# Kernel tuning notes

Measured on AMD Instinct MI355X. Metric: run time of the kernel, lower is better.

Reference implementation:

```python
import jax, jax.numpy as jnp
import numpy as np

V = 49688; D = 128; Hd = 256; DM = 2 * Hd; FF = 4 * Hd; NH = 4
B = 256; O = 32; L = 32

def _ln(x, g, b, eps=1e-5):
    m = x.mean(-1, keepdims=True)
    v = x.var(-1, keepdims=True)
    return (x - m) / jnp.sqrt(v + eps) * g + b

def _mha(x, in_w, in_b, out_w, out_b, nh):
    Bx, S, E = x.shape
    hd = E // nh
    qkv = x @ in_w.T + in_b
    q, k, v = jnp.split(qkv, 3, axis=-1)
    sp = lambda t: t.reshape(Bx, S, nh, hd).transpose(0, 2, 1, 3)
    q, k, v = sp(q), sp(k), sp(v)
    s = jnp.einsum('bhqd,bhkd->bhqk', q, k) / jnp.sqrt(jnp.asarray(hd, x.dtype))
    o = jnp.einsum('bhqk,bhkd->bhqd', jax.nn.softmax(s, -1), v)
    o = o.transpose(0, 2, 1, 3).reshape(Bx, S, E)
    return o @ out_w.T + out_b

def _gru_dir(x, wih, whh, bih, bhh):
    Bx, T, _ = x.shape
    H = whh.shape[1]
    def step(h, xt):
        gi = xt @ wih.T + bih
        gh = h @ whh.T + bhh
        ir, iz, inn = jnp.split(gi, 3, -1)
        hr, hz, hn = jnp.split(gh, 3, -1)
        r = jax.nn.sigmoid(ir + hr)
        z = jax.nn.sigmoid(iz + hz)
        n = jnp.tanh(inn + r * hn)
        h = (1 - z) * n + z * h
        return h, h
    _, hs = jax.lax.scan(step, jnp.zeros((Bx, H), x.dtype), jnp.swapaxes(x, 0, 1))
    return jnp.swapaxes(hs, 0, 1)

def setup_inputs():
    key = jax.random.key(0)
    it = iter(jax.random.split(key, 48))
    def nrm(shape, s=0.05):
        return jax.random.normal(next(it), shape, jnp.float32) * s
    inp = {}
    inp['order_history'] = jax.random.randint(next(it), (B, O, L), 0, V + 1)
    inp['days_between'] = jax.random.uniform(next(it), (B, O - 1), jnp.float32) * 30.0
    inp['days_since_last'] = jax.random.uniform(next(it), (B,), jnp.float32) * 30.0
    inp['emb'] = nrm((V + 1, D), 1.0).at[0].set(0.0)  # padding_idx=0 -> zero row
    inp['a_in_w'] = nrm((3 * D, D)); inp['a_in_b'] = jnp.zeros((3 * D,))
    inp['a_out_w'] = nrm((D, D)); inp['a_out_b'] = jnp.zeros((D,))
    for d in ('f', 'b'):
        inp['g_wih_' + d] = nrm((3 * Hd, D)); inp['g_whh_' + d] = nrm((3 * Hd, Hd))
        inp['g_bih_' + d] = jnp.zeros((3 * Hd,)); inp['g_bhh_' + d] = jnp.zeros((3 * Hd,))
    inp['t_in_w'] = nrm((3 * DM, DM)); inp['t_in_b'] = jnp.zeros((3 * DM,))
    inp['t_out_w'] = nrm((DM, DM)); inp['t_out_b'] = jnp.zeros((DM,))
    inp['t_ln1_g'] = jnp.ones((DM,)); inp['t_ln1_b'] = jnp.zeros((DM,))
    inp['t_ff1_w'] = nrm((FF, DM)); inp['t_ff1_b'] = jnp.zeros((FF,))
    inp['t_ff2_w'] = nrm((DM, FF)); inp['t_ff2_b'] = jnp.zeros((DM,))
    inp['t_ln2_g'] = jnp.ones((DM,)); inp['t_ln2_b'] = jnp.zeros((DM,))
    inp['te1_w'] = nrm((Hd // 4, 2)); inp['te1_b'] = jnp.zeros((Hd // 4,))
    inp['te_ln1_g'] = jnp.ones((Hd // 4,)); inp['te_ln1_b'] = jnp.zeros((Hd // 4,))
    inp['te2_w'] = nrm((Hd // 2, Hd // 4)); inp['te2_b'] = jnp.zeros((Hd // 2,))
    inp['te_ln2_g'] = jnp.ones((Hd // 2,)); inp['te_ln2_b'] = jnp.zeros((Hd // 2,))
    inp['c_w'] = nrm((Hd, 2 * Hd + Hd // 2)); inp['c_b'] = jnp.zeros((Hd,))
    inp['c_ln_g'] = jnp.ones((Hd,)); inp['c_ln_b'] = jnp.zeros((Hd,))
    return inp

def reference(order_history, days_between, days_since_last, emb, a_in_w, a_in_b, a_out_w, a_out_b, g_wih_f, g_whh_f, g_bih_f, g_bhh_f, g_wih_b, g_whh_b, g_bih_b, g_bhh_b, t_in_w, t_in_b, t_out_w, t_out_b, t_ln1_g, t_ln1_b, t_ff1_w, t_ff1_b, t_ff2_w, t_ff2_b, t_ln2_g, t_ln2_b, te1_w, te1_b, te_ln1_g, te_ln1_b, te2_w, te2_b, te_ln2_g, te_ln2_b, c_w, c_b, c_ln_g, c_ln_b):
    Bx, Ox, Lx = order_history.shape
    # per-order item self-attention, batched over all (user, order) pairs
    x = emb[order_history].reshape(Bx * Ox, Lx, -1)                  # [B*O, L, D]
    x = _mha(x, a_in_w, a_in_b, a_out_w, a_out_b, NH)
    order_emb = x.mean(1).reshape(Bx, Ox, -1)                        # [B, O, D]
    # bidirectional GRU over the order sequence
    hf = _gru_dir(order_emb, g_wih_f, g_whh_f, g_bih_f, g_bhh_f)
    hb = _gru_dir(order_emb[:, ::-1], g_wih_b, g_whh_b, g_bih_b, g_bhh_b)[:, ::-1]
    g = jnp.concatenate([hf, hb], -1)                                # [B, O, 2H]
    # post-LN TransformerEncoderLayer (relu, dropout in eval mode)
    a = _mha(g, t_in_w, t_in_b, t_out_w, t_out_b, NH)
    g = _ln(g + a, t_ln1_g, t_ln1_b)
    f = jax.nn.relu(g @ t_ff1_w.T + t_ff1_b) @ t_ff2_w.T + t_ff2_b
    g = _ln(g + f, t_ln2_g, t_ln2_b)
    enc = g.mean(1)                                                  # [B, 2H]
    # temporal features: only days_mean and recency are used (std computed but unused in original)
    feats = jnp.stack([days_between.mean(1), days_since_last], 1)    # [B, 2]
    te = jax.nn.relu(_ln(feats @ te1_w.T + te1_b, te_ln1_g, te_ln1_b))
    te = jax.nn.relu(_ln(te @ te2_w.T + te2_b, te_ln2_g, te_ln2_b))  # [B, H/2]
    out = jax.nn.relu(_ln(jnp.concatenate([enc, te], 1) @ c_w.T + c_b, c_ln_g, c_ln_b))
    return out                                                       # [B, H]
```

## Files before the change

### kernel.cpp

```cpp
#include <hip/hip_runtime.h>
#include <hip/hip_bf16.h>
#include <math.h>

typedef __hip_bfloat16 bf16;
typedef __attribute__((ext_vector_type(8))) short short8v;
typedef __attribute__((ext_vector_type(4))) short short4v;
typedef __attribute__((ext_vector_type(4))) float float4v;
#define MFMA16 __builtin_amdgcn_mfma_f32_16x16x32_bf16

__device__ __forceinline__ float us2f(unsigned short u) {
  union { unsigned u; float f; } c; c.u = ((unsigned)u) << 16; return c.f;
}
__device__ __forceinline__ unsigned short f2us(float f) {
  return __bfloat16_as_ushort(__float2bfloat16(f));
}

__device__ __forceinline__ float dot_ff(const float* __restrict__ x,
                                        const float* __restrict__ w, int K) {
  const float4* xp = reinterpret_cast<const float4*>(x);
  const float4* wp = reinterpret_cast<const float4*>(w);
  float acc = 0.f;
  const int n = K >> 2;
  for (int i = 0; i < n; ++i) {
    float4 a = xp[i], b = wp[i];
    acc += a.x*b.x + a.y*b.y + a.z*b.z + a.w*b.w;
  }
  return acc;
}

__device__ __forceinline__ float sigm(float x) { return 1.f / (1.f + __expf(-x)); }
__device__ __forceinline__ float tanh_fast(float x) {
  x = fminf(fmaxf(x, -15.f), 15.f);
  float e = __expf(2.f * x);
  return (e - 1.f) / (e + 1.f);
}

__global__ void k_canary(float* __restrict__ out) {
  out[blockIdx.x * 256 + threadIdx.x] = 100.0f;
}

__global__ __launch_bounds__(256) void k_cvt(
    const float* __restrict__ a_in_w, const float* __restrict__ t_in_w,
    const float* __restrict__ t_out_w, const float* __restrict__ t_ff1w,
    const float* __restrict__ t_ff2w, const float* __restrict__ a_out_w,
    const float* __restrict__ emb,
    unsigned short* __restrict__ awb, unsigned short* __restrict__ twb,
    unsigned short* __restrict__ pwb, unsigned short* __restrict__ f1wb,
    unsigned short* __restrict__ f2wb, unsigned short* __restrict__ awb2,
    unsigned short* __restrict__ embb)
{
  int i = blockIdx.x * 256 + threadIdx.x;
  if (i < 1590048) {
    float4 e4 = *reinterpret_cast<const float4*>(emb + (size_t)i * 4);
    short4v s; s[0] = f2us(e4.x); s[1] = f2us(e4.y); s[2] = f2us(e4.z); s[3] = f2us(e4.w);
    *reinterpret_cast<short4v*>(embb + (size_t)i * 4) = s;
  }
  if (i < 49152)  awb[i] = f2us(a_in_w[i]);
  if (i < 786432) twb[i] = f2us(t_in_w[i]);
  if (i < 262144) pwb[i] = f2us(t_out_w[i]);
  if (i < 524288) f1wb[i] = f2us(t_ff1w[i]);
  if (i < 524288) f2wb[i] = f2us(t_ff2w[i]);
  if (i < 16384)  awb2[i] = f2us(a_out_w[i]);
}

__global__ __launch_bounds__(256) void k_gru_wb(
    const float* __restrict__ wih_f, const float* __restrict__ whh_f,
    const float* __restrict__ wih_b, const float* __restrict__ whh_b,
    unsigned short* __restrict__ whhb, unsigned short* __restrict__ wihb)
{
  int i = blockIdx.x * 256 + threadIdx.x;
  if (i >= 393216) return;
  int dir = i / 196608, r = i % 196608;
  whhb[i] = f2us((dir ? whh_b : whh_f)[r]);
  if (r < 98304) wihb[dir * 98304 + r] = f2us((dir ? wih_b : wih_f)[r]);
}

__global__ __launch_bounds__(256, 5) void k_order_attn(
    const int* __restrict__ oh, const unsigned short* __restrict__ embb,
    const unsigned short* __restrict__ awb, const float* __restrict__ in_b,
    const unsigned short* __restrict__ awb2, const float* __restrict__ out_b,
    unsigned short* __restrict__ oeb)
{
  const int bo = blockIdx.x;
  const int tid = threadIdx.x;
  __shared__ alignas(16) unsigned short regA[32 * 136];
  __shared__ alignas(16) unsigned short qb[32 * 136];
  __shared__ alignas(16) unsigned short kb[32 * 136];
  unsigned short* xs = regA;
  unsigned short* vT = regA;
  unsigned short* ob = qb;
  unsigned short* pb = kb;

  const int lane = tid & 63, wave = tid >> 6;
  const int l15 = lane & 15, quad = lane >> 4;

  for (int i = tid; i < 512; i += 256) {
    int t = i >> 4, c8 = (i & 15) << 3;
    int id = oh[bo * 32 + t];
    *reinterpret_cast<short8v*>(xs + t * 136 + c8) =
        *reinterpret_cast<const short8v*>(embb + (size_t)id * 128 + c8);
  }
  __syncthreads();
  short8v af[2][4];
#pragma unroll
  for (int mt = 0; mt < 2; ++mt)
#pragma unroll
    for (int kc = 0; kc < 4; ++kc)
      af[mt][kc] = *reinterpret_cast<const short8v*>(
          xs + (mt * 16 + l15) * 136 + kc * 32 + quad * 8);
  __syncthreads();
  for (int ni = 0; ni < 6; ++ni) {
    const int j = (wave + ni * 4) * 16 + l15;
    const unsigned short* wrow = awb + (size_t)j * 128;
    float4v acc0 = {0.f, 0.f, 0.f, 0.f}, acc1 = {0.f, 0.f, 0.f, 0.f};
#pragma unroll
    for (int kc = 0; kc < 4; ++kc) {
      short8v bfr = *reinterpret_cast<const short8v*>(wrow + kc * 32 + quad * 8);
      acc0 = MFMA16(af[0][kc], bfr, acc0, 0, 0, 0);
      acc1 = MFMA16(af[1][kc], bfr, acc1, 0, 0, 0);
    }
    const float bj = in_b[j];
    const int jj = j & 127;
    if (j < 256) {
      unsigned short* dst = (j < 128) ? qb : kb;
#pragma unroll
      for (int r = 0; r < 4; ++r) {
        int t0 = quad * 4 + r;
        dst[t0 * 136 + jj] = f2us(acc0[r] + bj);
        dst[(t0 + 16) * 136 + jj] = f2us(acc1[r] + bj);
      }
    } else {
      short4v s0, s1;
#pragma unroll
      for (int r = 0; r < 4; ++r) { s0[r] = f2us(acc0[r] + bj); s1[r] = f2us(acc1[r] + bj); }
      *reinterpret_cast<short4v*>(vT + jj * 32 + quad * 4) = s0;
      *reinterpret_cast<short4v*>(vT + jj * 32 + 16 + quad * 4) = s1;
    }
  }
  __syncthreads();
  {
    const int h = wave;
    const float scale1 = 0.17677669529663687f;
    short8v qf[2], kf[2];
#pragma unroll
    for (int mt = 0; mt < 2; ++mt)
      qf[mt] = *reinterpret_cast<const short8v*>(qb + (mt * 16 + l15) * 136 + h * 32 + quad * 8);
#pragma unroll
    for (int nt = 0; nt < 2; ++nt)
      kf[nt] = *reinterpret_cast<const short8v*>(kb + (nt * 16 + l15) * 136 + h * 32 + quad * 8);
    float4v sacc[2][2];
#pragma unroll
    for (int mt = 0; mt < 2; ++mt)
#pragma unroll
      for (int nt = 0; nt < 2; ++nt) {
        sacc[mt][nt] = (float4v){0.f, 0.f, 0.f, 0.f};
        sacc[mt][nt] = MFMA16(qf[mt], kf[nt], sacc[mt][nt], 0, 0, 0);
      }
    __syncthreads();
#pragma unroll
    for (int mt = 0; mt < 2; ++mt)
#pragma unroll
      for (int r = 0; r < 4; ++r) {
        float e0 = __expf(sacc[mt][0][r] * scale1);
        float e1 = __expf(sacc[mt][1][r] * scale1);
        int row = h * 32 + mt * 16 + quad * 4 + r;
        pb[row * 32 + l15] = f2us(e0);
        pb[row * 32 + 16 + l15] = f2us(e1);
      }
    short8v ones;
#pragma unroll
    for (int i = 0; i < 8; ++i) ones[i] = (short)0x3F80;
    short8v pf[2], vf[2];
#pragma unroll
    for (int mt = 0; mt < 2; ++mt)
      pf[mt] = *reinterpret_cast<const short8v*>(pb + (h * 32 + mt * 16 + l15) * 32 + quad * 8);
    float4v sums[2];
#pragma unroll
    for (int mt = 0; mt < 2; ++mt) {
      sums[mt] = (float4v){0.f, 0.f, 0.f, 0.f};
      sums[mt] = MFMA16(pf[mt], ones, sums[mt], 0, 0, 0);
    }
#pragma unroll
    for (int nt = 0; nt < 2; ++nt)
      vf[nt] = *reinterpret_cast<const short8v*>(vT + (h * 32 + nt * 16 + l15) * 32 + quad * 8);
    float4v oacc[2][2];
#pragma unroll
    for (int mt = 0; mt < 2; ++mt)
#pragma unroll
      for (int nt = 0; nt < 2; ++nt) {
        oacc[mt][nt] = (float4v){0.f, 0.f, 0.f, 0.f};
        oacc[mt][nt] = MFMA16(pf[mt], vf[nt], oacc[mt][nt], 0, 0, 0);
      }
#pragma unroll
    for (int mt = 0; mt < 2; ++mt)
#pragma unroll
      for (int r = 0; r < 4; ++r) {
        int t = mt * 16 + quad * 4 + r;
        float inv = 1.f / sums[mt][r];
#pragma unroll
        for (int nt = 0; nt < 2; ++nt)
          ob[t * 136 + h * 32 + nt * 16 + l15] = f2us(oacc[mt][nt][r] * inv);
      }
  }
  __syncthreads();
  {
    float4v acc[2][2];
#pragma unroll
    for (int mt = 0; mt < 2; ++mt)
#pragma unroll
      for (int nt = 0; nt < 2; ++nt) acc[mt][nt] = (float4v){0.f, 0.f, 0.f, 0.f};
#pragma unroll
    for (int kc = 0; kc < 4; ++kc) {
      short8v af0 = *reinterpret_cast<const short8v*>(ob + l15 * 136 + kc * 32 + quad * 8);
      short8v af1 = *reinterpret_cast<const short8v*>(ob + (16 + l15) * 136 + kc * 32 + quad * 8);
#pragma unroll
      for (int nt = 0; nt < 2; ++nt) {
        int j = (wave * 2 + nt) * 16 + l15;
        short8v bfr = *reinterpret_cast<const short8v*>(awb2 + (size_t)j * 128 + kc * 32 + quad * 8);
        acc[0][nt] = MFMA16(af0, bfr, acc[0][nt], 0, 0, 0);
        acc[1][nt] = MFMA16(af1, bfr, acc[1][nt], 0, 0, 0);
      }
    }
#pragma unroll
    for (int nt = 0; nt < 2; ++nt) {
      float part = 0.f;
#pragma unroll
      for (int mt = 0; mt < 2; ++mt)
#pragma unroll
        for (int r = 0; r < 4; ++r) part += acc[mt][nt][r];
      part += __shfl_xor(part, 16);
      part += __shfl_xor(part, 32);
      if (quad == 0) {
        int j = (wave * 2 + nt) * 16 + l15;
        oeb[(size_t)bo * 128 + j] = f2us(part * (1.f / 32.f) + out_b[j]);
      }
    }
  }
}

__global__ __launch_bounds__(256, 2) void k_gru_gi(
    const unsigned short* __restrict__ oeb, const unsigned short* __restrict__ wihb,
    unsigned short* __restrict__ gi)
{
  const int row0 = blockIdx.x * 32, tid = threadIdx.x;
  __shared__ alignas(16) unsigned short xs[32 * 136];
  for (int i = tid; i < 512; i += 256) {
    int t = i >> 4, c8 = (i & 15) << 3;
    *reinterpret_cast<short8v*>(xs + t * 136 + c8) =
        *reinterpret_cast<const short8v*>(oeb + (size_t)(row0 + t) * 128 + c8);
  }
  __syncthreads();
  const int lane = tid & 63, wave = tid >> 6;
  const int l15 = lane & 15, quad = lane >> 4;
  short8v af[2][4];
#pragma unroll
  for (int mt = 0; mt < 2; ++mt)
#pragma unroll
    for (int kc = 0; kc < 4; ++kc)
      af[mt][kc] = *reinterpret_cast<const short8v*>(
          xs + (mt * 16 + l15) * 136 + kc * 32 + quad * 8);
  for (int ni = 0; ni < 24; ++ni) {
    int col = (wave + ni * 4) * 16 + l15;
    const unsigned short* wrow = wihb + (size_t)col * 128;
    float4v a0 = {0.f,0.f,0.f,0.f}, a1 = {0.f,0.f,0.f,0.f};
#pragma unroll
    for (int kc = 0; kc < 4; ++kc) {
      short8v bfr = *reinterpret_cast<const short8v*>(wrow + kc * 32 + quad * 8);
      a0 = MFMA16(af[0][kc], bfr, a0, 0, 0, 0);
      a1 = MFMA16(af[1][kc], bfr, a1, 0, 0, 0);
    }
#pragma unroll
    for (int r = 0; r < 4; ++r) {
      gi[(size_t)(row0 + quad * 4 + r) * 1536 + col] = f2us(a0[r]);
      gi[(size_t)(row0 + quad * 4 + r + 16) * 1536 + col] = f2us(a1[r]);
    }
  }
}

__global__ __launch_bounds__(512, 2) void k_gru_rec(
    const unsigned short* __restrict__ gi, const unsigned short* __restrict__ whhb,
    const float* __restrict__ bih_f, const float* __restrict__ bhh_f,
    const float* __restrict__ bih_b, const float* __restrict__ bhh_b,
    float* __restrict__ g)
{
  const int b0 = blockIdx.x * 2, dir = blockIdx.y;
  const int tid = threadIdx.x;
  const unsigned short* wb = whhb + (size_t)dir * 196608;
  const float* bih = dir ? bih_b : bih_f;
  const float* bhh = dir ? bhh_b : bhh_f;
  __shared__ alignas(16) unsigned short hb[16 * 264];
  __shared__ float pg[2 * 772];
  const int lane = tid & 63, wave = tid >> 6;
  const int l15 = lane & 15, quad = lane >> 4;
  const int j = tid & 255, mb = tid >> 8;
  const float bir = bih[j], biz = bih[256 + j], bin_ = bih[512 + j];
  const float bhr = bhh[j], bhz = bhh[256 + j], bhn  = bhh[512 + j];
  short8v wf[6][8];
  int cols[6];
#pragma unroll
  for (int ni = 0; ni < 6; ++ni) {
    cols[ni] = (wave + ni * 8) * 16 + l15;
#pragma unroll
    for (int kc = 0; kc < 8; ++kc)
      wf[ni][kc] = *reinterpret_cast<const short8v*>(
          wb + (size_t)cols[ni] * 256 + kc * 32 + quad * 8);
  }
  for (int i = tid; i < 16 * 264; i += 512) hb[i] = 0;
  int tcur = dir ? 31 : 0;
  size_t gbase = ((size_t)(b0 + mb) * 32 + tcur) * 1536 + dir * 768;
  float gr = us2f(gi[gbase + j]);
  float gz = us2f(gi[gbase + 256 + j]);
  float gn = us2f(gi[gbase + 512 + j]);
  __syncthreads();
  for (int s = 0; s < 32; ++s) {
    float4v acc[6];
#pragma unroll
    for (int ni = 0; ni < 6; ++ni) acc[ni] = (float4v){0.f, 0.f, 0.f, 0.f};
#pragma unroll
    for (int kc = 0; kc < 8; ++kc) {
      short8v af = *reinterpret_cast<const short8v*>(hb + l15 * 264 + kc * 32 + quad * 8);
#pragma unroll
      for (int ni = 0; ni < 6; ++ni)
        acc[ni] = MFMA16(af, wf[ni][kc], acc[ni], 0, 0, 0);
    }
    if (quad == 0) {
#pragma unroll
      for (int ni = 0; ni < 6; ++ni) {
        pg[cols[ni]] = acc[ni][0];
        pg[772 + cols[ni]] = acc[ni][1];
      }
    }
    float gr2 = 0.f, gz2 = 0.f, gn2 = 0.f;
    if (s < 31) {
      int t2 = dir ? (30 - s) : (s + 1);
      size_t gb2 = ((size_t)(b0 + mb) * 32 + t2) * 1536 + dir * 768;
      gr2 = us2f(gi[gb2 + j]);
      gz2 = us2f(gi[gb2 + 256 + j]);
      gn2 = us2f(gi[gb2 + 512 + j]);
    }
    __syncthreads();
    {
      const int tt = dir ? (31 - s) : s;
      float hprev = us2f(hb[mb * 264 + j]);
      float r = sigm(gr + bir + pg[mb * 772 + j] + bhr);
      float z = sigm(gz + biz + pg[mb * 772 + 256 + j] + bhz);
      float n = tanh_fast(gn + bin_ + r * (pg[mb * 772 + 512 + j] + bhn));
      float nh = (1.f - z) * n + z * hprev;
      hb[mb * 264 + j] = f2us(nh);
      g[((size_t)(b0 + mb) * 32 + tt) * 512 + dir * 256 + j] = nh;
    }
    gr = gr2; gz = gz2; gn = gn2;
    __syncthreads();
  }
}

__global__ __launch_bounds__(256, 4) void k_mha2f(
    const float* __restrict__ g, const unsigned short* __restrict__ twb,
    const float* __restrict__ Bv, float* __restrict__ attn)
{
  const int b = blockIdx.x, h = blockIdx.y, tid = threadIdx.x;
  __shared__ alignas(16) unsigned short xs3[32 * 136];
  __shared__ alignas(16) unsigned short qk[2 * 32 * 136];
  __shared__ alignas(16) unsigned short vT[128 * 40];
  unsigned short* qs = qk;
  unsigned short* ks = qk + 32 * 136;
  unsigned short* pb = xs3;
  const int lane = tid & 63, wave = tid >> 6;
  const int l15 = lane & 15, quad = lane >> 4;

  int wrowi[6];
#pragma unroll
  for (int ni = 0; ni < 6; ++ni) {
    int idx = (wave + ni * 4) * 16 + l15;
    int m = idx >> 7, dd = idx & 127;
    wrowi[ni] = m * 512 + h * 128 + dd;
  }
  float4v acc[6][2];
#pragma unroll
  for (int ni = 0; ni < 6; ++ni)
#pragma unroll
    for (int mt = 0; mt < 2; ++mt) acc[ni][mt] = (float4v){0.f, 0.f, 0.f, 0.f};

  for (int ck = 0; ck < 4; ++ck) {
    __syncthreads();
    for (int i = tid; i < 1024; i += 256) {
      int t = i >> 5, c4 = (i & 31) << 2;
      float4 e4 = *reinterpret_cast<const float4*>(
          g + (size_t)b * 16384 + t * 512 + ck * 128 + c4);
      short4v s; s[0] = f2us(e4.x); s[1] = f2us(e4.y); s[2] = f2us(e4.z); s[3] = f2us(e4.w);
      *reinterpret_cast<short4v*>(xs3 + t * 136 + c4) = s;
    }
    __syncthreads();
    short8v af2[2][4];
#pragma unroll
    for (int mt = 0; mt < 2; ++mt)
#pragma unroll
      for (int u = 0; u < 4; ++u)
        af2[mt][u] = *reinterpret_cast<const short8v*>(
            xs3 + (mt * 16 + l15) * 136 + u * 32 + quad * 8);
#pragma unroll
    for (int ni = 0; ni < 6; ++ni) {
      const unsigned short* wrow = twb + (size_t)wrowi[ni] * 512 + ck * 128;
#pragma unroll
      for (int u = 0; u < 4; ++u) {
        short8v bfr = *reinterpret_cast<const short8v*>(wrow + u * 32 + quad * 8);
        acc[ni][0] = MFMA16(af2[0][u], bfr, acc[ni][0], 0, 0, 0);
        acc[ni][1] = MFMA16(af2[1][u], bfr, acc[ni][1], 0, 0, 0);
      }
    }
  }
  __syncthreads();
#pragma unroll
  for (int ni = 0; ni < 6; ++ni) {
    int idx = (wave + ni * 4) * 16 + l15;
    int m = idx >> 7, dd = idx & 127;
    float bj = Bv[wrowi[ni]];
    if (m < 2) {
      unsigned short* dst = (m == 0) ? qs : ks;
#pragma unroll
      for (int r = 0; r < 4; ++r) {
        int t0 = quad * 4 + r;
        dst[t0 * 136 + dd] = f2us(acc[ni][0][r] + bj);
        dst[(t0 + 16) * 136 + dd] = f2us(acc[ni][1][r] + bj);
      }
    } else {
      short4v s0, s1;
#pragma unroll
      for (int r = 0; r < 4; ++r) { s0[r] = f2us(acc[ni][0][r] + bj); s1[r] = f2us(acc[ni][1][r] + bj); }
      *reinterpret_cast<short4v*>(vT + dd * 40 + quad * 4) = s0;
      *reinterpret_cast<short4v*>(vT + dd * 40 + 16 + quad * 4) = s1;
    }
  }
  __syncthreads();
  {
    const float scale2 = 0.08838834764831845f;
    const int mt = wave >> 1, nt = wave & 1;
    float4v a = {0.f, 0.f, 0.f, 0.f};
#pragma unroll
    for (int kc = 0; kc < 4; ++kc) {
      short8v qf = *reinterpret_cast<const short8v*>(qs + (mt * 16 + l15) * 136 + kc * 32 + quad * 8);
      short8v kf = *reinterpret_cast<const short8v*>(ks + (nt * 16 + l15) * 136 + kc * 32 + quad * 8);
      a = MFMA16(qf, kf, a, 0, 0, 0);
    }
#pragma unroll
    for (int r = 0; r < 4; ++r) {
      int row = mt * 16 + quad * 4 + r;
      pb[row * 32 + nt * 16 + l15] = f2us(__expf(a[r] * scale2));
    }
  }
  __syncthreads();
  {
    short8v ones;
#pragma unroll
    for (int i = 0; i < 8; ++i) ones[i] = (short)0x3F80;
    short8v pf[2], vf[2];
#pragma unroll
    for (int mt = 0; mt < 2; ++mt)
      pf[mt] = *reinterpret_cast<const short8v*>(pb + (mt * 16 + l15) * 32 + quad * 8);
    float4v sums[2];
#pragma unroll
    for (int mt = 0; mt < 2; ++mt) {
      sums[mt] = (float4v){0.f, 0.f, 0.f, 0.f};
      sums[mt] = MFMA16(pf[mt], ones, sums[mt], 0, 0, 0);
    }
#pragma unroll
    for (int ntl = 0; ntl < 2; ++ntl)
      vf[ntl] = *reinterpret_cast<const short8v*>(vT + ((2 * wave + ntl) * 16 + l15) * 40 + quad * 8);
    float4v oacc[2][2];
#pragma unroll
    for (int mt = 0; mt < 2; ++mt)
#pragma unroll
      for (int ntl = 0; ntl < 2; ++ntl) {
        oacc[mt][ntl] = (float4v){0.f, 0.f, 0.f, 0.f};
        oacc[mt][ntl] = MFMA16(pf[mt], vf[ntl], oacc[mt][ntl], 0, 0, 0);
      }
#pragma unroll
    for (int mt = 0; mt < 2; ++mt)
#pragma unroll
      for (int r = 0; r < 4; ++r) {
        int q = mt * 16 + quad * 4 + r;
        float inv = 1.f / sums[mt][r];
#pragma unroll
        for (int ntl = 0; ntl < 2; ++ntl)
          attn[((size_t)b * 32 + q) * 512 + h * 128 + (2 * wave + ntl) * 16 + l15] =
              oacc[mt][ntl][r] * inv;
      }
  }
}

__global__ __launch_bounds__(512, 2) void k_projln_mfma(
    const float* __restrict__ X, const unsigned short* __restrict__ Wb,
    const float* __restrict__ bias, const float* __restrict__ res,
    const float* __restrict__ gam, const float* __restrict__ bet,
    float* __restrict__ Y)
{
  const int row0 = blockIdx.x * 16, tid = threadIdx.x;
  __shared__ alignas(16) unsigned short xs[16 * 520];
  __shared__ float ys[16 * 516];
  for (int i = tid; i < 16 * 512; i += 512) {
    int t = i >> 9, c = i & 511;
    xs[t * 520 + c] = f2us(X[(size_t)(row0 + t) * 512 + c]);
  }
  __syncthreads();
  {
    const int lane = tid & 63, wave = tid >> 6;
    const int l15 = lane & 15, quad = lane >> 4;
    short8v af[16];
#pragma unroll
    for (int kc = 0; kc < 16; ++kc)
      af[kc] = *reinterpret_cast<const short8v*>(xs + l15 * 520 + kc * 32 + quad * 8);
    for (int ni = 0; ni < 4; ++ni) {
      int col = (wave + ni * 8) * 16 + l15;
      const unsigned short* wrow = Wb + (size_t)col * 512;
      float4v acc = {0.f,0.f,0.f,0.f};
#pragma unroll
      for (int kc = 0; kc < 16; ++kc) {
        short8v bfr = *reinterpret_cast<const short8v*>(wrow + kc * 32 + quad * 8);
        acc = MFMA16(af[kc], bfr, acc, 0, 0, 0);
      }
      float bj = bias[col];
#pragma unroll
      for (int r = 0; r < 4; ++r)
        ys[(quad * 4 + r) * 516 + col] = acc[r] + bj;
    }
  }
  __syncthreads();
  for (int i = tid; i < 16 * 512; i += 512) {
    int t = i >> 9, c = i & 511;
    ys[t * 516 + c] += res[(size_t)(row0 + t) * 512 + c];
  }
  __syncthreads();
  {
    int row = tid >> 5, l32 = tid & 31;
    const float* yr = ys + row * 516;
    float part = 0.f;
#pragma unroll
    for (int k = 0; k < 16; ++k) part += yr[l32 + 32 * k];
#pragma unroll
    for (int off = 16; off; off >>= 1) part += __shfl_xor(part, off, 32);
    float mean = part * (1.f / 512.f);
    float var = 0.f;
#pragma unroll
    for (int k = 0; k < 16; ++k) { float d = yr[l32 + 32 * k] - mean; var += d * d; }
#pragma unroll
    for (int off = 16; off; off >>= 1) var += __shfl_xor(var, off, 32);
    float rs = rsqrtf(var * (1.f / 512.f) + 1e-5f);
    for (int k = 0; k < 16; ++k) {
      int c = l32 + 32 * k;
      Y[(size_t)(row0 + row) * 512 + c] = (yr[c] - mean) * rs * gam[c] + bet[c];
    }
  }
}

__global__ __launch_bounds__(512, 2) void k_ffln(
    const float* __restrict__ X, const unsigned short* __restrict__ W1,
    const float* __restrict__ b1, const unsigned short* __restrict__ W2,
    const float* __restrict__ b2, const float* __restrict__ res,
    const float* __restrict__ gam, const float* __restrict__ bet,
    float* __restrict__ Y)
{
  const int row0 = blockIdx.x * 16, tid = threadIdx.x;
  __shared__ alignas(16) unsigned short xs[16 * 520];
  __shared__ alignas(16) unsigned short f1L[16 * 1032];
  float* ys = reinterpret_cast<float*>(f1L);
  const int lane = tid & 63, wave = tid >> 6;
  const int l15 = lane & 15, quad = lane >> 4;
  for (int i = tid; i < 16 * 512; i += 512) {
    int t = i >> 9, c = i & 511;
    xs[t * 520 + c] = f2us(X[(size_t)(row0 + t) * 512 + c]);
  }
  __syncthreads();
  for (int ni = 0; ni < 8; ++ni) {
    int col = (wave + ni * 8) * 16 + l15;
    const unsigned short* wrow = W1 + (size_t)col * 512;
    float4v acc = {0.f,0.f,0.f,0.f};
#pragma unroll
    for (int kc = 0; kc < 16; ++kc) {
      short8v a = *reinterpret_cast<const short8v*>(xs + l15 * 520 + kc * 32 + quad * 8);
      short8v bfr = *reinterpret_cast<const short8v*>(wrow + kc * 32 + quad * 8);
      acc = MFMA16(a, bfr, acc, 0, 0, 0);
    }
    float bj = b1[col];
#pragma unroll
    for (int r = 0; r < 4; ++r)
      f1L[(quad * 4 + r) * 1032 + col] = f2us(fmaxf(acc[r] + bj, 0.f));
  }
  __syncthreads();
  float4v acc2[4];
#pragma unroll
  for (int ni = 0; ni < 4; ++ni) acc2[ni] = (float4v){0.f,0.f,0.f,0.f};
  int cols2[4];
#pragma unroll
  for (int ni = 0; ni < 4; ++ni) cols2[ni] = (wave + ni * 8) * 16 + l15;
  for (int half = 0; half < 2; ++half) {
    for (int kc = 0; kc < 16; ++kc) {
      short8v a = *reinterpret_cast<const short8v*>(
          f1L + l15 * 1032 + half * 512 + kc * 32 + quad * 8);
#pragma unroll
      for (int ni = 0; ni < 4; ++ni) {
        short8v bfr = *reinterpret_cast<const short8v*>(
            W2 + (size_t)cols2[ni] * 1024 + half * 512 + kc * 32 + quad * 8);
        acc2[ni] = MFMA16(a, bfr, acc2[ni], 0, 0, 0);
      }
    }
  }
  __syncthreads();
  for (int ni = 0; ni < 4; ++ni) {
    int col = cols2[ni];
    float bj = b2[col];
#pragma unroll
    for (int r = 0; r < 4; ++r)
      ys[(quad * 4 + r) * 516 + col] = acc2[ni][r] + bj;
  }
  __syncthreads();
  for (int i = tid; i < 16 * 512; i += 512) {
    int t = i >> 9, c = i & 511;
    ys[t * 516 + c] += res[(size_t)(row0 + t) * 512 + c];
  }
  __syncthreads();
  {
    int row = tid >> 5, l32 = tid & 31;
    const float* yr = ys + row * 516;
    float part = 0.f;
#pragma unroll
    for (int k = 0; k < 16; ++k) part += yr[l32 + 32 * k];
#pragma unroll
    for (int off = 16; off; off >>= 1) part += __shfl_xor(part, off, 32);
    float mean = part * (1.f / 512.f);
    float var = 0.f;
#pragma unroll
    for (int k = 0; k < 16; ++k) { float d = yr[l32 + 32 * k] - mean; var += d * d; }
#pragma unroll
    for (int off = 16; off; off >>= 1) var += __shfl_xor(var, off, 32);
    float rs = rsqrtf(var * (1.f / 512.f) + 1e-5f);
    for (int k = 0; k < 16; ++k) {
      int c = l32 + 32 * k;
      Y[(size_t)(row0 + row) * 512 + c] = (yr[c] - mean) * rs * gam[c] + bet[c];
    }
  }
}

__global__ __launch_bounds__(256) void k_final(
    const float* __restrict__ g2,
    const float* __restrict__ db, const float* __restrict__ dsl,
    const float* __restrict__ te1_w, const float* __restrict__ te1_b,
    const float* __restrict__ l1g, const float* __restrict__ l1b,
    const float* __restrict__ te2_w, const float* __restrict__ te2_b,
    const float* __restrict__ l2g, const float* __restrict__ l2b,
    const float* __restrict__ c_w, const float* __restrict__ c_b,
    const float* __restrict__ clg, const float* __restrict__ clb,
    float* __restrict__ out)
{
  const int b = blockIdx.x, tid = threadIdx.x;
  __shared__ float cat[640];
  __shared__ float t1[64];
  __shared__ float t2[128];
  __shared__ float pre[256];
  __shared__ float red[256];
  __shared__ float st[2];
  for (int i = tid; i < 512; i += 256) {
    float acc = 0.f;
#pragma unroll
    for (int t = 0; t < 32; ++t) acc += g2[((size_t)b * 32 + t) * 512 + i];
    cat[i] = acc * (1.f / 32.f);
  }
  if (tid == 0) {
    float s = 0.f;
    for (int i = 0; i < 31; ++i) s += db[b * 31 + i];
    st[0] = s / 31.f;
    st[1] = dsl[b];
  }
  __syncthreads();
  const float f0 = st[0], f1v = st[1];
  if (tid < 64)
    t1[tid] = f0 * te1_w[tid * 2] + f1v * te1_w[tid * 2 + 1] + te1_b[tid];
  __syncthreads();
  if (tid == 0) {
    float m = 0.f; for (int i = 0; i < 64; ++i) m += t1[i]; m *= (1.f / 64.f);
    float v = 0.f; for (int i = 0; i < 64; ++i) { float d = t1[i] - m; v += d * d; }
    st[0] = m; st[1] = rsqrtf(v * (1.f / 64.f) + 1e-5f);
  }
  __syncthreads();
  if (tid < 64) {
    float v = (t1[tid] - st[0]) * st[1] * l1g[tid] + l1b[tid];
    t1[tid] = fmaxf(v, 0.f);
  }
  __syncthreads();
  if (tid < 128)
    t2[tid] = dot_ff(t1, te2_w + (size_t)tid * 64, 64) + te2_b[tid];
  __syncthreads();
  if (tid == 0) {
    float m = 0.f; for (int i = 0; i < 128; ++i) m += t2[i]; m *= (1.f / 128.f);
    float v = 0.f; for (int i = 0; i < 128; ++i) { float d = t2[i] - m; v += d * d; }
    st[0] = m; st[1] = rsqrtf(v * (1.f / 128.f) + 1e-5f);
  }
  __syncthreads();
  if (tid < 128) {
    float v = (t2[tid] - st[0]) * st[1] * l2g[tid] + l2b[tid];
    cat[512 + tid] = fmaxf(v, 0.f);
  }
  __syncthreads();
  pre[tid] = dot_ff(cat, c_w + (size_t)tid * 640, 640) + c_b[tid];
  red[tid] = pre[tid];
  __syncthreads();
  for (int s = 128; s > 0; s >>= 1) { if (tid < s) red[tid] += red[tid + s]; __syncthreads(); }
  const float m = red[0] * (1.f / 256.f);
  __syncthreads();
  const float d = pre[tid] - m;
  red[tid] = d * d;
  __syncthreads();
  for (int s = 128; s > 0; s >>= 1) { if (tid < s) red[tid] += red[tid + s]; __syncthreads(); }
  const float rs = rsqrtf(red[0] * (1.f / 256.f) + 1e-5f);
  float v = d * rs * clg[tid] + clb[tid];
  out[(size_t)b * 256 + tid] = fmaxf(v, 0.f);
}

extern "C" void kernel_launch(void* const* d_in, const int* in_sizes, int n_in,
                              void* d_out, int out_size, void* d_ws, size_t ws_size,
                              hipStream_t stream) {
  (void)in_sizes; (void)n_in; (void)out_size; (void)ws_size;
  const int*   oh     = (const int*)  d_in[0];
  const float* db     = (const float*)d_in[1];
  const float* dsl    = (const float*)d_in[2];
  const float* emb    = (const float*)d_in[3];
  const float* a_in_w = (const float*)d_in[4];
  const float* a_in_b = (const float*)d_in[5];
  const float* a_out_w= (const float*)d_in[6];
  const float* a_out_b= (const float*)d_in[7];
  const float* wih_f  = (const float*)d_in[8];
  const float* whh_f  = (const float*)d_in[9];
  const float* bih_f  = (const float*)d_in[10];
  const float* bhh_f  = (const float*)d_in[11];
  const float* wih_b  = (const float*)d_in[12];
  const float* whh_b  = (const float*)d_in[13];
  const float* bih_b  = (const float*)d_in[14];
  const float* bhh_b  = (const float*)d_in[15];
  const float* t_in_w = (const float*)d_in[16];
  const float* t_in_b = (const float*)d_in[17];
  const float* t_out_w= (const float*)d_in[18];
  const float* t_out_b= (const float*)d_in[19];
  const float* t_ln1g = (const float*)d_in[20];
  const float* t_ln1b = (const float*)d_in[21];
  const float* t_ff1w = (const float*)d_in[22];
  const float* t_ff1b = (const float*)d_in[23];
  const float* t_ff2w = (const float*)d_in[24];
  const float* t_ff2b = (const float*)d_in[25];
  const float* t_ln2g = (const float*)d_in[26];
  const float* t_ln2b = (const float*)d_in[27];
  const float* te1_w  = (const float*)d_in[28];
  const float* te1_b  = (const float*)d_in[29];
  const float* tl1g   = (const float*)d_in[30];
  const float* tl1b   = (const float*)d_in[31];
  const float* te2_w  = (const float*)d_in[32];
  const float* te2_b  = (const float*)d_in[33];
  const float* tl2g   = (const float*)d_in[34];
  const float* tl2b   = (const float*)d_in[35];
  const float* c_w    = (const float*)d_in[36];
  const float* c_b    = (const float*)d_in[37];
  const float* clng   = (const float*)d_in[38];
  const float* clnb   = (const float*)d_in[39];

  float* ws = (float*)d_ws;
  unsigned short* oeb = (unsigned short*)ws;
  unsigned short* embb= (unsigned short*)(ws + 1048576);
  float* g    = ws + 1048576;
  float* attn = ws + 5242880;
  float* g1   = attn;
  float* g2   = attn;
  unsigned short* whhb = (unsigned short*)(ws + 9437184);
  unsigned short* wihb = (unsigned short*)(ws + 9633792);
  unsigned short* awb2 = (unsigned short*)(ws + 9732096);
  unsigned short* awb  = (unsigned short*)(ws + 10027008);
  unsigned short* twb  = (unsigned short*)(ws + 10051584);
  unsigned short* pwb  = (unsigned short*)(ws + 10444800);
  unsigned short* f1wb = (unsigned short*)(ws + 10575872);
  unsigned short* f2wb = (unsigned short*)(ws + 10838016);
  unsigned short* gi   = (unsigned short*)(ws + 11100160);

  k_canary<<<256, 256, 0, stream>>>((float*)d_out);
  k_cvt<<<6212, 256, 0, stream>>>(a_in_w, t_in_w, t_out_w, t_ff1w, t_ff2w, a_out_w,
                                  emb, awb, twb, pwb, f1wb, f2wb, awb2, embb);
  k_gru_wb<<<1536, 256, 0, stream>>>(wih_f, whh_f, wih_b, whh_b, whhb, wihb);
  k_order_attn<<<8192, 256, 0, stream>>>(oh, embb, awb, a_in_b, awb2, a_out_b, oeb);
  k_gru_gi<<<256, 256, 0, stream>>>(oeb, wihb, gi);
  k_gru_rec<<<dim3(128, 2), 512, 0, stream>>>(gi, whhb, bih_f, bhh_f, bih_b, bhh_b, g);
  k_mha2f<<<dim3(256, 4), 256, 0, stream>>>(g, twb, t_in_b, attn);
  k_projln_mfma<<<512, 512, 0, stream>>>(attn, pwb, t_out_b, g, t_ln1g, t_ln1b, g1);
  k_ffln<<<512, 512, 0, stream>>>(g1, f1wb, t_ff1b, f2wb, t_ff2b, g1,
                                  t_ln2g, t_ln2b, g2);
  k_final<<<256, 256, 0, stream>>>(g2, db, dsl, te1_w, te1_b, tl1g, tl1b,
                                   te2_w, te2_b, tl2g, tl2b, c_w, c_b, clng, clnb,
                                   (float*)d_out);
}
```

Baseline: 601.4 us.

## Precompute QKV projection per vocabulary row instead of per gathered token

The QKV input projection is moved out of the per-order attention kernel into a new kernel that projects every embedding row once, fused with the fp32-to-bf16 embedding conversion. The attention kernel then gathers precomputed Q/K and V rows by token id and transposes V into shared memory. This replaces 262K token projections with about 50K vocabulary-row projections, at the cost of writing and gathering wider rows (384 bf16 values instead of 128). Work spent on vocabulary rows that never appear is wasted, and the V transpose now uses scalar shared-memory stores.

```diff
diff --git a/kernel.cpp b/kernel.cpp
--- a/kernel.cpp
+++ b/kernel.cpp
@@ -43,18 +43,11 @@
     const float* __restrict__ a_in_w, const float* __restrict__ t_in_w,
     const float* __restrict__ t_out_w, const float* __restrict__ t_ff1w,
     const float* __restrict__ t_ff2w, const float* __restrict__ a_out_w,
-    const float* __restrict__ emb,
     unsigned short* __restrict__ awb, unsigned short* __restrict__ twb,
     unsigned short* __restrict__ pwb, unsigned short* __restrict__ f1wb,
-    unsigned short* __restrict__ f2wb, unsigned short* __restrict__ awb2,
-    unsigned short* __restrict__ embb)
+    unsigned short* __restrict__ f2wb, unsigned short* __restrict__ awb2)
 {
   int i = blockIdx.x * 256 + threadIdx.x;
-  if (i < 1590048) {
-    float4 e4 = *reinterpret_cast<const float4*>(emb + (size_t)i * 4);
-    short4v s; s[0] = f2us(e4.x); s[1] = f2us(e4.y); s[2] = f2us(e4.z); s[3] = f2us(e4.w);
-    *reinterpret_cast<short4v*>(embb + (size_t)i * 4) = s;
-  }
   if (i < 49152)  awb[i] = f2us(a_in_w[i]);
   if (i < 786432) twb[i] = f2us(t_in_w[i]);
   if (i < 262144) pwb[i] = f2us(t_out_w[i]);
@@ -75,32 +68,23 @@
   if (r < 98304) wihb[dir * 98304 + r] = f2us((dir ? wih_b : wih_f)[r]);
 }
 
-__global__ __launch_bounds__(256, 5) void k_order_attn(
-    const int* __restrict__ oh, const unsigned short* __restrict__ embb,
-    const unsigned short* __restrict__ awb, const float* __restrict__ in_b,
-    const unsigned short* __restrict__ awb2, const float* __restrict__ out_b,
-    unsigned short* __restrict__ oeb)
-{
-  const int bo = blockIdx.x;
-  const int tid = threadIdx.x;
-  __shared__ alignas(16) unsigned short regA[32 * 136];
-  __shared__ alignas(16) unsigned short qb[32 * 136];
-  __shared__ alignas(16) unsigned short kb[32 * 136];
-  unsigned short* xs = regA;
-  unsigned short* vT = regA;
-  unsigned short* ob = qb;
-  unsigned short* pb = kb;
-
+__global__ __launch_bounds__(256, 2) void k_qkvpre(
+    const float* __restrict__ emb, const unsigned short* __restrict__ awb,
+    const float* __restrict__ in_b,
+    unsigned short* __restrict__ qkt, unsigned short* __restrict__ vt)
+{
+  const int row0 = blockIdx.x * 32, tid = threadIdx.x;
+  __shared__ alignas(16) unsigned short xs[32 * 136];
+  for (int i = tid; i < 1024; i += 256) {
+    int t = i >> 5, c4 = (i & 31) << 2;
+    int grow = row0 + t; if (grow > 49688) grow = 49688;
+    float4 e4 = *reinterpret_cast<const float4*>(emb + (size_t)grow * 128 + c4);
+    short4v s; s[0] = f2us(e4.x); s[1] = f2us(e4.y); s[2] = f2us(e4.z); s[3] = f2us(e4.w);
+    *reinterpret_cast<short4v*>(xs + t * 136 + c4) = s;
+  }
+  __syncthreads();
   const int lane = tid & 63, wave = tid >> 6;
   const int l15 = lane & 15, quad = lane >> 4;
-
-  for (int i = tid; i < 512; i += 256) {
-    int t = i >> 4, c8 = (i & 15) << 3;
-    int id = oh[bo * 32 + t];
-    *reinterpret_cast<short8v*>(xs + t * 136 + c8) =
-        *reinterpret_cast<const short8v*>(embb + (size_t)id * 128 + c8);
-  }
-  __syncthreads();
   short8v af[2][4];
 #pragma unroll
   for (int mt = 0; mt < 2; ++mt)
@@ -108,7 +92,6 @@
     for (int kc = 0; kc < 4; ++kc)
       af[mt][kc] = *reinterpret_cast<const short8v*>(
           xs + (mt * 16 + l15) * 136 + kc * 32 + quad * 8);
-  __syncthreads();
   for (int ni = 0; ni < 6; ++ni) {
     const int j = (wave + ni * 4) * 16 + l15;
     const unsigned short* wrow = awb + (size_t)j * 128;
@@ -120,22 +103,51 @@
       acc1 = MFMA16(af[1][kc], bfr, acc1, 0, 0, 0);
     }
     const float bj = in_b[j];
-    const int jj = j & 127;
-    if (j < 256) {
-      unsigned short* dst = (j < 128) ? qb : kb;
-#pragma unroll
-      for (int r = 0; r < 4; ++r) {
-        int t0 = quad * 4 + r;
-        dst[t0 * 136 + jj] = f2us(acc0[r] + bj);
-        dst[(t0 + 16) * 136 + jj] = f2us(acc1[r] + bj);
-      }
-    } else {
-      short4v s0, s1;
-#pragma unroll
-      for (int r = 0; r < 4; ++r) { s0[r] = f2us(acc0[r] + bj); s1[r] = f2us(acc1[r] + bj); }
-      *reinterpret_cast<short4v*>(vT + jj * 32 + quad * 4) = s0;
-      *reinterpret_cast<short4v*>(vT + jj * 32 + 16 + quad * 4) = s1;
-    }
+#pragma unroll
+    for (int r = 0; r < 4; ++r) {
+      int g0 = row0 + quad * 4 + r, g1 = g0 + 16;
+      if (j < 256) {
+        if (g0 <= 49688) qkt[(size_t)g0 * 256 + j] = f2us(acc0[r] + bj);
+        if (g1 <= 49688) qkt[(size_t)g1 * 256 + j] = f2us(acc1[r] + bj);
+      } else {
+        int jj = j - 256;
+        if (g0 <= 49688) vt[(size_t)g0 * 128 + jj] = f2us(acc0[r] + bj);
+        if (g1 <= 49688) vt[(size_t)g1 * 128 + jj] = f2us(acc1[r] + bj);
+      }
+    }
+  }
+}
+
+__global__ __launch_bounds__(256, 5) void k_order_attn(
+    const int* __restrict__ oh, const unsigned short* __restrict__ qkt,
+    const unsigned short* __restrict__ vt,
+    const unsigned short* __restrict__ awb2, const float* __restrict__ out_b,
+    unsigned short* __restrict__ oeb)
+{
+  const int bo = blockIdx.x;
+  const int tid = threadIdx.x;
+  __shared__ alignas(16) unsigned short qb[32 * 136];
+  __shared__ alignas(16) unsigned short kb[32 * 136];
+  __shared__ alignas(16) unsigned short vTb[128 * 32];
+  unsigned short* ob = qb;
+  unsigned short* pb = kb;
+
+  const int lane = tid & 63, wave = tid >> 6;
+  const int l15 = lane & 15, quad = lane >> 4;
+
+  for (int i = tid; i < 1024; i += 256) {
+    int t = i >> 5, c8 = (i & 31) << 3;
+    int id = oh[bo * 32 + t];
+    short8v v8 = *reinterpret_cast<const short8v*>(qkt + (size_t)id * 256 + c8);
+    if (c8 < 128) *reinterpret_cast<short8v*>(qb + t * 136 + c8) = v8;
+    else          *reinterpret_cast<short8v*>(kb + t * 136 + (c8 - 128)) = v8;
+  }
+  for (int i = tid; i < 512; i += 256) {
+    int t = i >> 4, c8 = (i & 15) << 3;
+    int id = oh[bo * 32 + t];
+    short8v v8 = *reinterpret_cast<const short8v*>(vt + (size_t)id * 128 + c8);
+#pragma unroll
+    for (int j2 = 0; j2 < 8; ++j2) vTb[(c8 + j2) * 32 + t] = v8[j2];
   }
   __syncthreads();
   {
@@ -182,7 +194,7 @@
     }
 #pragma unroll
     for (int nt = 0; nt < 2; ++nt)
-      vf[nt] = *reinterpret_cast<const short8v*>(vT + (h * 32 + nt * 16 + l15) * 32 + quad * 8);
+      vf[nt] = *reinterpret_cast<const short8v*>(vTb + (h * 32 + nt * 16 + l15) * 32 + quad * 8);
     float4v oacc[2][2];
 #pragma unroll
     for (int mt = 0; mt < 2; ++mt)
@@ -761,8 +773,8 @@
   const float* clnb   = (const float*)d_in[39];
 
   float* ws = (float*)d_ws;
-  unsigned short* oeb = (unsigned short*)ws;
-  unsigned short* embb= (unsigned short*)(ws + 1048576);
+  unsigned short* oeb  = (unsigned short*)ws;
+  unsigned short* qkt  = (unsigned short*)(ws + 1048576);
   float* g    = ws + 1048576;
   float* attn = ws + 5242880;
   float* g1   = attn;
@@ -775,13 +787,15 @@
   unsigned short* pwb  = (unsigned short*)(ws + 10444800);
   unsigned short* f1wb = (unsigned short*)(ws + 10575872);
   unsigned short* f2wb = (unsigned short*)(ws + 10838016);
+  unsigned short* vt   = (unsigned short*)(ws + 11100160);
   unsigned short* gi   = (unsigned short*)(ws + 11100160);
 
   k_canary<<<256, 256, 0, stream>>>((float*)d_out);
-  k_cvt<<<6212, 256, 0, stream>>>(a_in_w, t_in_w, t_out_w, t_ff1w, t_ff2w, a_out_w,
-                                  emb, awb, twb, pwb, f1wb, f2wb, awb2, embb);
+  k_cvt<<<3072, 256, 0, stream>>>(a_in_w, t_in_w, t_out_w, t_ff1w, t_ff2w, a_out_w,
+                                  awb, twb, pwb, f1wb, f2wb, awb2);
   k_gru_wb<<<1536, 256, 0, stream>>>(wih_f, whh_f, wih_b, whh_b, whhb, wihb);
-  k_order_attn<<<8192, 256, 0, stream>>>(oh, embb, awb, a_in_b, awb2, a_out_b, oeb);
+  k_qkvpre<<<1553, 256, 0, stream>>>(emb, awb, a_in_b, qkt, vt);
+  k_order_attn<<<8192, 256, 0, stream>>>(oh, qkt, vt, awb2, a_out_b, oeb);
   k_gru_gi<<<256, 256, 0, stream>>>(oeb, wihb, gi);
   k_gru_rec<<<dim3(128, 2), 512, 0, stream>>>(gi, whhb, bih_f, bhh_f, bih_b, bhh_b, g);
   k_mha2f<<<dim3(256, 4), 256, 0, stream>>>(g, twb, t_in_b, attn);
```

After: 575.1 us. 4.4% less time.
